# Performance work log

Measured on AMD Instinct MI355X. Metric: run time of the kernel, lower is better.

The kernel has to match this reference:

```python
import jax, jax.numpy as jnp
import numpy as np

HEADS = 8
DIM_HEAD = 64
SCALE = DIM_HEAD ** -0.5


def setup_inputs() -> dict:
    key = jax.random.key(0)
    k1, k2, k3 = jax.random.split(key, 3)
    b, dim, n = 4, 256, 2048
    hidden = HEADS * DIM_HEAD  # 512
    x = jax.random.normal(k1, (b, dim, n), dtype=jnp.float32)
    # Conv1d kernel-size-1 weights are pointwise linear maps over channels.
    w_qkv = jax.random.normal(k2, (3 * hidden, dim), dtype=jnp.float32) * (dim ** -0.5)
    w_out = jax.random.normal(k3, (dim, hidden), dtype=jnp.float32) * (hidden ** -0.5)
    b_out = jnp.zeros((dim,), dtype=jnp.float32)
    return {"x": x, "w_qkv": w_qkv, "w_out": w_out, "b_out": b_out}


def reference(x, w_qkv, w_out, b_out):
    b, dim, n = x.shape
    hidden = w_out.shape[1]
    # pointwise conv1d == channel matmul: [3h, dim] x [b, dim, n] -> [b, 3h, n]
    qkv = jnp.einsum('oi,bin->bon', w_qkv, x)
    q, k, v = jnp.split(qkv, 3, axis=1)
    # b (h c) n -> b h c n
    reshape = lambda t: t.reshape(b, HEADS, DIM_HEAD, n)
    q, k, v = reshape(q) * SCALE, reshape(k), reshape(v)
    sim = jnp.einsum('bhdi,bhdj->bhij', q, k)          # [b, h, n, n]
    attn = jax.nn.softmax(sim, axis=-1)
    out = jnp.einsum('bhij,bhdj->bhid', attn, v)        # [b, h, n, d]
    # b h n d -> b (h d) n
    out = out.transpose(0, 1, 3, 2).reshape(b, hidden, n)
    return jnp.einsum('oi,bin->bon', w_out, out) + b_out[None, :, None]
```

## Files before the change

### kernel.cpp

```cpp
#include <hip/hip_runtime.h>
#include <stdint.h>

#define SEQ  2048
#define DIMC 256
#define HID  512
#define NH   8
#define DH   64

typedef __attribute__((ext_vector_type(8))) short bf16x8;
typedef __attribute__((ext_vector_type(4))) float f32x4;
typedef __attribute__((ext_vector_type(16))) float f32x16;
typedef __attribute__((ext_vector_type(2))) unsigned uint2v;
typedef __attribute__((address_space(1))) const uint32_t guint_t;
typedef __attribute__((address_space(3))) uint32_t luint_t;

__device__ __forceinline__ void gld16(const void* g, void* l) {
  __builtin_amdgcn_global_load_lds((guint_t*)g, (luint_t*)l, 16, 0, 0);
}

__device__ __forceinline__ void barrier_raw() {
  asm volatile("" ::: "memory");
  __builtin_amdgcn_s_barrier();
  asm volatile("" ::: "memory");
}
#define WAITVM(n) asm volatile("s_waitcnt vmcnt(" #n ")" ::: "memory")

__device__ __forceinline__ unsigned short f2bf(float f) {
  union { float f; uint32_t u; } v; v.f = f;
  return (unsigned short)((v.u + 0x7FFFu + ((v.u >> 16) & 1u)) >> 16);
}

__device__ __forceinline__ uint32_t fbits(float f) {
  union { float f; uint32_t u; } v; v.f = f; return v.u;
}

__device__ __forceinline__ uint32_t pku(uint32_t u0, uint32_t u1) {
  return __builtin_amdgcn_perm(u1 + 0x8000u, u0 + 0x8000u, 0x07060302u);
}

__device__ __forceinline__ void swap32(uint32_t& a, uint32_t& b) {
#if __has_builtin(__builtin_amdgcn_permlane32_swap)
  uint2v r = __builtin_amdgcn_permlane32_swap(a, b, false, false);
  a = r[0]; b = r[1];
#else
  uint32_t aw = __shfl_xor(a, 32);
  uint32_t bw = __shfl_xor(b, 32);
  bool lo = (threadIdx.x & 32) == 0;
  uint32_t an = lo ? a : bw;
  uint32_t bn = lo ? aw : b;
  a = an; b = bn;
#endif
}

__global__ __launch_bounds__(256) void prep_kernel(
    const float* __restrict__ x, const float* __restrict__ wqkv,
    const float* __restrict__ wout,
    unsigned short* __restrict__ wqkv_b, unsigned short* __restrict__ wout_b,
    unsigned short* __restrict__ xT) {
  __shared__ float tile[64][65];
  int blk = blockIdx.x;
  int t = threadIdx.x;
  if (blk < 384) {
    int idx = blk * 1024 + t * 4;
    float4 v = *(const float4*)(wqkv + idx);
    float s = ((idx >> 8) < HID) ? 0.18033688011112042f : 1.0f;
    ushort4 o;
    o.x = f2bf(v.x * s); o.y = f2bf(v.y * s);
    o.z = f2bf(v.z * s); o.w = f2bf(v.w * s);
    *(ushort4*)(wqkv_b + idx) = o;
    return;
  }
  if (blk < 512) {
    int idx = (blk - 384) * 1024 + t * 4;
    float4 v = *(const float4*)(wout + idx);
    ushort4 o;
    o.x = f2bf(v.x); o.y = f2bf(v.y); o.z = f2bf(v.z); o.w = f2bf(v.w);
    *(ushort4*)(wout_b + idx) = o;
    return;
  }
  int tid = blk - 512;
  int b  = tid >> 7;
  int r  = tid & 127;
  int i0 = (r >> 5) * 64;
  int n0 = (r & 31) * 64;
  const float* xb = x + (size_t)b * DIMC * SEQ;
  int tn = t & 15, ti = t >> 4;
#pragma unroll
  for (int j = 0; j < 4; j++) {
    int il = ti + j * 16;
    float4 v = *(const float4*)(xb + (size_t)(i0 + il) * SEQ + n0 + tn * 4);
    tile[il][tn*4+0] = v.x; tile[il][tn*4+1] = v.y;
    tile[il][tn*4+2] = v.z; tile[il][tn*4+3] = v.w;
  }
  __syncthreads();
  unsigned short* xTb = xT + (size_t)b * SEQ * DIMC;
#pragma unroll
  for (int j = 0; j < 4; j++) {
    int nl = ti + j * 16;
    int i4 = tn * 4;
    uint2 pk;
    pk.x = (uint32_t)f2bf(tile[i4+0][nl]) | ((uint32_t)f2bf(tile[i4+1][nl]) << 16);
    pk.y = (uint32_t)f2bf(tile[i4+2][nl]) | ((uint32_t)f2bf(tile[i4+3][nl]) << 16);
    *(uint2*)(xTb + (size_t)(n0 + nl) * DIMC + i0 + i4) = pk;
  }
}

__global__ __launch_bounds__(256, 2) void qkv_gemm(
    const unsigned short* __restrict__ wq, const unsigned short* __restrict__ xT,
    unsigned short* __restrict__ Qs, unsigned short* __restrict__ Ks,
    unsigned short* __restrict__ Vt) {
  __shared__ unsigned short lds[32768];
  int o0 = blockIdx.x * 128;
  int n0 = blockIdx.y * 128;
  int b  = blockIdx.z;
  int t  = threadIdx.x;
  int wv = t >> 6, l = t & 63, l15 = l & 15, q = l >> 4;
  int wm = (wv & 1) * 64, wn = (wv >> 1) * 64;
  f32x4 acc[4][4];
#pragma unroll
  for (int i = 0; i < 4; i++)
#pragma unroll
    for (int j = 0; j < 4; j++) acc[i][j] = (f32x4){0.f, 0.f, 0.f, 0.f};
  const unsigned short* Ag = wq + (size_t)o0 * DIMC;
  const unsigned short* Bg = xT + ((size_t)b * SEQ + n0) * DIMC;
  int lrow8 = l >> 3, lcol = l & 7;

  auto stage = [&](int kk, int buf) {
    unsigned short* la = lds + (buf << 14);
    unsigned short* lb = la + 8192;
    int k0 = kk * 64;
#pragma unroll
    for (int c0 = 0; c0 < 4; c0++) {
      int c = wv * 4 + c0;
      int row = c * 8 + lrow8;
      int sg = lcol ^ (row & 7);
      gld16(Ag + (size_t)row * DIMC + k0 + sg * 8, la + c * 512);
      gld16(Bg + (size_t)row * DIMC + k0 + sg * 8, lb + c * 512);
    }
  };

  stage(0, 0);
  for (int kk = 0; kk < 4; kk++) {
    int cur = kk & 1;
    WAITVM(0);
    barrier_raw();
    if (kk < 3) stage(kk + 1, cur ^ 1);
    unsigned short* la = lds + (cur << 14);
    unsigned short* lb = la + 8192;
#pragma unroll
    for (int kh = 0; kh < 2; kh++) {
      bf16x8 af[4], bfr[4];
#pragma unroll
      for (int mt = 0; mt < 4; mt++) {
        int row = wm + mt*16 + l15;
        af[mt] = *(const bf16x8*)(la + row*64 + ((kh*4 + q) ^ (row & 7)) * 8);
      }
#pragma unroll
      for (int nt = 0; nt < 4; nt++) {
        int row = wn + nt*16 + l15;
        bfr[nt] = *(const bf16x8*)(lb + row*64 + ((kh*4 + q) ^ (row & 7)) * 8);
      }
#pragma unroll
      for (int mt = 0; mt < 4; mt++)
#pragma unroll
        for (int nt = 0; nt < 4; nt++)
          acc[mt][nt] = __builtin_amdgcn_mfma_f32_16x16x32_bf16(af[mt], bfr[nt], acc[mt][nt], 0, 0, 0);
    }
  }
  barrier_raw();
  int seg3 = o0 >> 9;
  int h0   = (o0 & 511) >> 6;
  if (seg3 == 2) {
#pragma unroll
    for (int mt = 0; mt < 4; mt++)
#pragma unroll
      for (int nt = 0; nt < 4; nt++)
#pragma unroll
        for (int r = 0; r < 4; r++) {
          int ol = wm + mt * 16 + q * 4 + r;
          int h = h0 + (ol >> 6), d = ol & 63;
          int n = n0 + wn + nt * 16 + l15;
          Vt[(((size_t)b * NH + h) * DH + d) * SEQ + n] = f2bf(acc[mt][nt][r]);
        }
  } else {
    unsigned short* dst = (seg3 == 0) ? Qs : Ks;
#pragma unroll
    for (int mt = 0; mt < 4; mt++)
#pragma unroll
      for (int nt = 0; nt < 4; nt++)
#pragma unroll
        for (int r = 0; r < 4; r++) {
          int ol = wm + mt * 16 + q * 4 + r;
          int nn = wn + nt * 16 + l15;
          lds[nn * 136 + ol] = f2bf(acc[mt][nt][r]);
        }
    __syncthreads();
#pragma unroll
    for (int i = 0; i < 8; i++) {
      int idx = i * 256 + t;
      int nn  = idx >> 4;
      int olb = (idx & 15) * 8;
      uint4 v = *(const uint4*)(lds + nn * 136 + olb);
      int h = h0 + (olb >> 6), d = olb & 63;
      *(uint4*)(dst + (((size_t)b * NH + h) * SEQ + n0 + nn) * DH + d) = v;
    }
  }
}

__global__ __launch_bounds__(256, 4) void attn_kernel(
    const unsigned short* __restrict__ Qs, const unsigned short* __restrict__ Ks,
    const unsigned short* __restrict__ Vt, unsigned short* __restrict__ AO) {
  __shared__ unsigned short KVs[16384];
  __shared__ float Lc[128];
  int id = blockIdx.x;
  int s  = id >> 3;
  int bh = (id & 7) * 4 + (s & 3);
  int q0 = (s >> 2) * 64;
  int b = bh >> 3, h = bh & 7;
  int t = threadIdx.x;
  int w = t >> 6, l = t & 63, l31 = l & 31, lh = l >> 5;
  int cg = w & 1, qg = w >> 1;
  const unsigned short* Qg = Qs + ((size_t)bh * SEQ + q0 + qg * 32) * DH;
  bf16x8 qb[4];
#pragma unroll
  for (int kc = 0; kc < 4; kc++)
    qb[kc] = *(const bf16x8*)(Qg + l31 * DH + kc*16 + lh*8);
  f32x16 oacc[2];
  float lsum = 0.f;
#pragma unroll
  for (int dt = 0; dt < 2; dt++)
#pragma unroll
    for (int r = 0; r < 16; r++) oacc[dt][r] = 0.f;

  const unsigned short* Ksrc = Ks + ((size_t)bh * SEQ + cg * 1024) * DH;
  const unsigned short* Vsrc = Vt + (size_t)bh * DH * SEQ + cg * 1024;

  auto stage = [&](int it2, int buf) {
    int jb = it2 * 32;
    unsigned short* base = KVs + buf * 8192;
    if (w < 2) {
      const unsigned short* src = Ksrc + (size_t)jb * DH;
      unsigned short* dst = base + cg * 2048;
#pragma unroll
      for (int g = 0; g < 4; g++) {
        int kr = g * 8 + (l >> 3);
        gld16(src + (size_t)kr * DH + ((l & 7) ^ (kr & 7)) * 8, dst + g * 512);
      }
    } else {
      const unsigned short* src = Vsrc + jb;
      unsigned short* dst = base + 4096 + cg * 2048;
#pragma unroll
      for (int g = 0; g < 4; g++) {
        int r = g * 8 + (l >> 3);
        int u = (l & 7) ^ (r & 7);
        int d = (u >> 2) * 32 + r;
        int j = u & 3;
        gld16(src + (size_t)d * SEQ + j * 8, dst + g * 512);
      }
    }
  };

  stage(0, 0);
  for (int it = 0; it < 32; it++) {
    int cur = it & 1;
    WAITVM(0);
    barrier_raw();
    if (it < 31) stage(it + 1, cur ^ 1);
    const unsigned short* Kst = KVs + cur * 8192 + cg * 2048;
    const unsigned short* Vst = KVs + cur * 8192 + 4096 + cg * 2048;
    f32x16 st;
#pragma unroll
    for (int r = 0; r < 16; r++) st[r] = 0.f;
#pragma unroll
    for (int kc = 0; kc < 4; kc++) {
      bf16x8 kf = *(const bf16x8*)(Kst + l31 * 64 + ((kc*2 + lh) ^ (l31 & 7)) * 8);
      st = __builtin_amdgcn_mfma_f32_32x32x16_bf16(kf, qb[kc], st, 0, 0, 0);
    }
    bf16x8 vf[2][2];
#pragma unroll
    for (int kc2 = 0; kc2 < 2; kc2++)
#pragma unroll
      for (int dt = 0; dt < 2; dt++)
        vf[kc2][dt] = *(const bf16x8*)(Vst + l31 * 64 +
                                       ((dt*4 + kc2*2 + lh) ^ (l31 & 7)) * 8);
    float p[16];
    float s0 = 0.f;
#pragma unroll
    for (int r = 0; r < 16; r++) { p[r] = __builtin_amdgcn_exp2f(st[r]); s0 += p[r]; }
    lsum += s0;
    bf16x8 af[2];
#pragma unroll
    for (int hf = 0; hf < 2; hf++) {
      uint32_t xs[4], ys[4];
#pragma unroll
      for (int j = 0; j < 4; j++) {
        xs[j] = fbits(p[hf*8 + j]);
        ys[j] = fbits(p[hf*8 + 4 + j]);
        swap32(xs[j], ys[j]);
      }
      uint32_t d0 = pku(xs[0], xs[1]);
      uint32_t d1 = pku(xs[2], xs[3]);
      uint32_t d2 = pku(ys[0], ys[1]);
      uint32_t d3 = pku(ys[2], ys[3]);
      union { uint32_t u[4]; bf16x8 v; } cv;
      cv.u[0] = d0; cv.u[1] = d1; cv.u[2] = d2; cv.u[3] = d3;
      af[hf] = cv.v;
    }
#pragma unroll
    for (int kc2 = 0; kc2 < 2; kc2++)
#pragma unroll
      for (int dt = 0; dt < 2; dt++)
        oacc[dt] = __builtin_amdgcn_mfma_f32_32x32x16_bf16(af[kc2], vf[kc2][dt], oacc[dt], 0, 0, 0);
  }
  {
    float v = lsum;
    v += __shfl_xor(v, 32);
    if (l < 32) Lc[cg * 64 + qg * 32 + l31] = v;
  }
  __syncthreads();
  float* Oc = (float*)KVs;
  if (cg == 1) {
#pragma unroll
    for (int dt = 0; dt < 2; dt++)
#pragma unroll
      for (int r = 0; r < 16; r++) {
        int qrow = qg*32 + (r & 3) + 8*(r >> 2) + 4*lh;
        Oc[qrow * 64 + dt*32 + l31] = oacc[dt][r];
      }
  }
  __syncthreads();
  if (cg == 0) {
    unsigned short* AOb = AO + (size_t)b * SEQ * HID + h * DH;
#pragma unroll
    for (int r = 0; r < 16; r++) {
      int qrow = qg*32 + (r & 3) + 8*(r >> 2) + 4*lh;
      float inv = __builtin_amdgcn_rcpf(Lc[qrow] + Lc[64 + qrow]);
      int n = q0 + qrow;
#pragma unroll
      for (int dt = 0; dt < 2; dt++) {
        float val = (oacc[dt][r] + Oc[qrow * 64 + dt*32 + l31]) * inv;
        AOb[(size_t)n * HID + dt*32 + l31] = f2bf(val);
      }
    }
  }
}

__global__ __launch_bounds__(256, 2) void out_gemm(
    const unsigned short* __restrict__ wo, const unsigned short* __restrict__ AO,
    const float* __restrict__ bias, float* __restrict__ out) {
  __shared__ unsigned short lds[24576];
  int o0 = blockIdx.x * 64;
  int n0 = blockIdx.y * 128;
  int b  = blockIdx.z;
  int t  = threadIdx.x;
  int wv = t >> 6, l = t & 63, l15 = l & 15, q = l >> 4;
  int wm = (wv & 1) * 32, wn = (wv >> 1) * 64;
  f32x4 acc[2][4];
#pragma unroll
  for (int i = 0; i < 2; i++)
#pragma unroll
    for (int j = 0; j < 4; j++) acc[i][j] = (f32x4){0.f,0.f,0.f,0.f};
  const unsigned short* Ag = wo + (size_t)o0 * HID;
  const unsigned short* Bg = AO + ((size_t)b * SEQ + n0) * HID;
  int lrow8 = l >> 3, lcol = l & 7;

  auto stage = [&](int kk, int buf) {
    unsigned short* la = lds + buf * 12288;
    unsigned short* lb = la + 4096;
    int k0 = kk * 64;
#pragma unroll
    for (int c0 = 0; c0 < 2; c0++) {
      int c = wv * 2 + c0;
      int row = c * 8 + lrow8;
      int sg = lcol ^ (row & 7);
      gld16(Ag + (size_t)row * HID + k0 + sg * 8, la + c * 512);
    }
#pragma unroll
    for (int c0 = 0; c0 < 4; c0++) {
      int c = wv * 4 + c0;
      int row = c * 8 + lrow8;
      int sg = lcol ^ (row & 7);
      gld16(Bg + (size_t)row * HID + k0 + sg * 8, lb + c * 512);
    }
  };

  stage(0, 0);
  for (int kk = 0; kk < 8; kk++) {
    int cur = kk & 1;
    WAITVM(0);
    barrier_raw();
    if (kk < 7) stage(kk + 1, cur ^ 1);
    unsigned short* la = lds + cur * 12288;
    unsigned short* lb = la + 4096;
#pragma unroll
    for (int kh = 0; kh < 2; kh++) {
      bf16x8 af[2], bfr[4];
#pragma unroll
      for (int mt = 0; mt < 2; mt++) {
        int row = wm + mt*16 + l15;
        af[mt] = *(const bf16x8*)(la + row*64 + ((kh*4 + q) ^ (row & 7)) * 8);
      }
#pragma unroll
      for (int nt = 0; nt < 4; nt++) {
        int row = wn + nt*16 + l15;
        bfr[nt] = *(const bf16x8*)(lb + row*64 + ((kh*4 + q) ^ (row & 7)) * 8);
      }
#pragma unroll
      for (int mt = 0; mt < 2; mt++)
#pragma unroll
        for (int nt = 0; nt < 4; nt++)
          acc[mt][nt] = __builtin_amdgcn_mfma_f32_16x16x32_bf16(af[mt], bfr[nt], acc[mt][nt], 0,0,0);
    }
  }
#pragma unroll
  for (int mt = 0; mt < 2; mt++)
#pragma unroll
    for (int nt = 0; nt < 4; nt++)
#pragma unroll
      for (int r = 0; r < 4; r++) {
        int o2 = o0 + wm + mt*16 + q*4 + r;
        int n  = n0 + wn + nt*16 + l15;
        out[((size_t)b * DIMC + o2) * SEQ + n] = acc[mt][nt][r] + bias[o2];
      }
}

extern "C" void kernel_launch(void* const* d_in, const int* in_sizes, int n_in,
                              void* d_out, int out_size, void* d_ws, size_t ws_size,
                              hipStream_t stream) {
  const float* x    = (const float*)d_in[0];
  const float* wqkv = (const float*)d_in[1];
  const float* wout = (const float*)d_in[2];
  const float* bout = (const float*)d_in[3];
  float* out = (float*)d_out;
  char* ws = (char*)d_ws;
  unsigned short* wqkv_b = (unsigned short*)(ws);
  unsigned short* wout_b = (unsigned short*)(ws + 786432);
  unsigned short* xT     = (unsigned short*)(ws + 1048576);
  unsigned short* Qs     = (unsigned short*)(ws + 5242880);
  unsigned short* Ks     = (unsigned short*)(ws + 13631488);
  unsigned short* Vt     = (unsigned short*)(ws + 22020096);
  unsigned short* AO     = (unsigned short*)(ws + 30408704);
  prep_kernel<<<1024, 256, 0, stream>>>(x, wqkv, wout, wqkv_b, wout_b, xT);
  qkv_gemm<<<dim3(12, 16, 4), 256, 0, stream>>>(wqkv_b, xT, Qs, Ks, Vt);
  attn_kernel<<<1024, 256, 0, stream>>>(Qs, Ks, Vt, AO);
  out_gemm<<<dim3(4, 16, 4), 256, 0, stream>>>(wout_b, AO, bout, out);
}
```

Before: 139.1 us.

## Tune attention inner loop, coalesce V stores, shrink out_gemm tiles

```diff
diff --git a/kernel.cpp b/kernel.cpp
--- a/kernel.cpp
+++ b/kernel.cpp
@@ -33,9 +33,14 @@
 __device__ __forceinline__ uint32_t fbits(float f) {
   union { float f; uint32_t u; } v; v.f = f; return v.u;
 }
-
-__device__ __forceinline__ uint32_t pku(uint32_t u0, uint32_t u1) {
-  return __builtin_amdgcn_perm(u1 + 0x8000u, u0 + 0x8000u, 0x07060302u);
+__device__ __forceinline__ float ffrombits(uint32_t u) {
+  union { uint32_t u; float f; } v; v.u = u; return v.f;
+}
+
+__device__ __forceinline__ uint32_t cvtpk(float a, float b) {
+  uint32_t r;
+  asm("v_cvt_pk_bf16_f32 %0, %1, %2" : "=v"(r) : "v"(a), "v"(b));
+  return r;
 }
 
 __device__ __forceinline__ void swap32(uint32_t& a, uint32_t& b) {
@@ -105,7 +110,7 @@
   }
 }
 
-__global__ __launch_bounds__(256, 2) void qkv_gemm(
+__global__ __launch_bounds__(256, 3) void qkv_gemm(
     const unsigned short* __restrict__ wq, const unsigned short* __restrict__ xT,
     unsigned short* __restrict__ Qs, unsigned short* __restrict__ Ks,
     unsigned short* __restrict__ Vt) {
@@ -178,10 +183,19 @@
 #pragma unroll
         for (int r = 0; r < 4; r++) {
           int ol = wm + mt * 16 + q * 4 + r;
-          int h = h0 + (ol >> 6), d = ol & 63;
-          int n = n0 + wn + nt * 16 + l15;
-          Vt[(((size_t)b * NH + h) * DH + d) * SEQ + n] = f2bf(acc[mt][nt][r]);
+          int nn = wn + nt * 16 + l15;
+          lds[ol * 136 + nn] = f2bf(acc[mt][nt][r]);
         }
+    __syncthreads();
+#pragma unroll
+    for (int i = 0; i < 8; i++) {
+      int idx = i * 256 + t;
+      int ol  = idx >> 4;
+      int nnb = (idx & 15) * 8;
+      uint4 v = *(const uint4*)(lds + ol * 136 + nnb);
+      int h = h0 + (ol >> 6), d = ol & 63;
+      *(uint4*)(Vt + (((size_t)b * NH + h) * DH + d) * SEQ + n0 + nnb) = v;
+    }
   } else {
     unsigned short* dst = (seg3 == 0) ? Qs : Ks;
 #pragma unroll
@@ -235,29 +249,36 @@
   const unsigned short* Ksrc = Ks + ((size_t)bh * SEQ + cg * 1024) * DH;
   const unsigned short* Vsrc = Vt + (size_t)bh * DH * SEQ + cg * 1024;
 
+  const unsigned short* sgp[4];
+  unsigned short* dst0;
+  size_t step;
+  if (w < 2) {
+#pragma unroll
+    for (int g = 0; g < 4; g++) {
+      int kr = g * 8 + (l >> 3);
+      sgp[g] = Ksrc + (size_t)kr * DH + ((l & 7) ^ (kr & 7)) * 8;
+    }
+    dst0 = (unsigned short*)KVs + cg * 2048;
+    step = (size_t)32 * DH;
+  } else {
+#pragma unroll
+    for (int g = 0; g < 4; g++) {
+      int r = g * 8 + (l >> 3);
+      int u = (l & 7) ^ (r & 7);
+      int d = (u >> 2) * 32 + r;
+      int j = u & 3;
+      sgp[g] = Vsrc + (size_t)d * SEQ + j * 8;
+    }
+    dst0 = (unsigned short*)KVs + 4096 + cg * 2048;
+    step = 32;
+  }
+
   auto stage = [&](int it2, int buf) {
-    int jb = it2 * 32;
-    unsigned short* base = KVs + buf * 8192;
-    if (w < 2) {
-      const unsigned short* src = Ksrc + (size_t)jb * DH;
-      unsigned short* dst = base + cg * 2048;
-#pragma unroll
-      for (int g = 0; g < 4; g++) {
-        int kr = g * 8 + (l >> 3);
-        gld16(src + (size_t)kr * DH + ((l & 7) ^ (kr & 7)) * 8, dst + g * 512);
-      }
-    } else {
-      const unsigned short* src = Vsrc + jb;
-      unsigned short* dst = base + 4096 + cg * 2048;
-#pragma unroll
-      for (int g = 0; g < 4; g++) {
-        int r = g * 8 + (l >> 3);
-        int u = (l & 7) ^ (r & 7);
-        int d = (u >> 2) * 32 + r;
-        int j = u & 3;
-        gld16(src + (size_t)d * SEQ + j * 8, dst + g * 512);
-      }
-    }
+    size_t off = (size_t)it2 * step;
+    unsigned short* dstb = dst0 + buf * 8192;
+#pragma unroll
+    for (int g = 0; g < 4; g++)
+      gld16(sgp[g] + off, dstb + g * 512);
   };
 
   stage(0, 0);
@@ -271,11 +292,13 @@
     f32x16 st;
 #pragma unroll
     for (int r = 0; r < 16; r++) st[r] = 0.f;
+    __builtin_amdgcn_s_setprio(1);
 #pragma unroll
     for (int kc = 0; kc < 4; kc++) {
       bf16x8 kf = *(const bf16x8*)(Kst + l31 * 64 + ((kc*2 + lh) ^ (l31 & 7)) * 8);
       st = __builtin_amdgcn_mfma_f32_32x32x16_bf16(kf, qb[kc], st, 0, 0, 0);
     }
+    __builtin_amdgcn_s_setprio(0);
     bf16x8 vf[2][2];
 #pragma unroll
     for (int kc2 = 0; kc2 < 2; kc2++)
@@ -284,10 +307,14 @@
         vf[kc2][dt] = *(const bf16x8*)(Vst + l31 * 64 +
                                        ((dt*4 + kc2*2 + lh) ^ (l31 & 7)) * 8);
     float p[16];
-    float s0 = 0.f;
-#pragma unroll
-    for (int r = 0; r < 16; r++) { p[r] = __builtin_amdgcn_exp2f(st[r]); s0 += p[r]; }
-    lsum += s0;
+#pragma unroll
+    for (int r = 0; r < 16; r++) p[r] = __builtin_amdgcn_exp2f(st[r]);
+    {
+      float t0 = p[0]+p[1],  t1 = p[2]+p[3],  t2 = p[4]+p[5],  t3 = p[6]+p[7];
+      float t4 = p[8]+p[9],  t5 = p[10]+p[11], t6 = p[12]+p[13], t7 = p[14]+p[15];
+      float u0 = t0+t1, u1 = t2+t3, u2 = t4+t5, u3 = t6+t7;
+      lsum += (u0+u1) + (u2+u3);
+    }
     bf16x8 af[2];
 #pragma unroll
     for (int hf = 0; hf < 2; hf++) {
@@ -298,19 +325,20 @@
         ys[j] = fbits(p[hf*8 + 4 + j]);
         swap32(xs[j], ys[j]);
       }
-      uint32_t d0 = pku(xs[0], xs[1]);
-      uint32_t d1 = pku(xs[2], xs[3]);
-      uint32_t d2 = pku(ys[0], ys[1]);
-      uint32_t d3 = pku(ys[2], ys[3]);
       union { uint32_t u[4]; bf16x8 v; } cv;
-      cv.u[0] = d0; cv.u[1] = d1; cv.u[2] = d2; cv.u[3] = d3;
+      cv.u[0] = cvtpk(ffrombits(xs[0]), ffrombits(xs[1]));
+      cv.u[1] = cvtpk(ffrombits(xs[2]), ffrombits(xs[3]));
+      cv.u[2] = cvtpk(ffrombits(ys[0]), ffrombits(ys[1]));
+      cv.u[3] = cvtpk(ffrombits(ys[2]), ffrombits(ys[3]));
       af[hf] = cv.v;
     }
+    __builtin_amdgcn_s_setprio(1);
 #pragma unroll
     for (int kc2 = 0; kc2 < 2; kc2++)
 #pragma unroll
       for (int dt = 0; dt < 2; dt++)
         oacc[dt] = __builtin_amdgcn_mfma_f32_32x32x16_bf16(af[kc2], vf[kc2][dt], oacc[dt], 0, 0, 0);
+    __builtin_amdgcn_s_setprio(0);
   }
   {
     float v = lsum;
@@ -348,24 +376,24 @@
 __global__ __launch_bounds__(256, 2) void out_gemm(
     const unsigned short* __restrict__ wo, const unsigned short* __restrict__ AO,
     const float* __restrict__ bias, float* __restrict__ out) {
-  __shared__ unsigned short lds[24576];
+  __shared__ unsigned short lds[16384];
   int o0 = blockIdx.x * 64;
-  int n0 = blockIdx.y * 128;
+  int n0 = blockIdx.y * 64;
   int b  = blockIdx.z;
   int t  = threadIdx.x;
   int wv = t >> 6, l = t & 63, l15 = l & 15, q = l >> 4;
-  int wm = (wv & 1) * 32, wn = (wv >> 1) * 64;
-  f32x4 acc[2][4];
+  int wm = (wv & 1) * 32, wn = (wv >> 1) * 32;
+  f32x4 acc[2][2];
 #pragma unroll
   for (int i = 0; i < 2; i++)
 #pragma unroll
-    for (int j = 0; j < 4; j++) acc[i][j] = (f32x4){0.f,0.f,0.f,0.f};
+    for (int j = 0; j < 2; j++) acc[i][j] = (f32x4){0.f,0.f,0.f,0.f};
   const unsigned short* Ag = wo + (size_t)o0 * HID;
   const unsigned short* Bg = AO + ((size_t)b * SEQ + n0) * HID;
   int lrow8 = l >> 3, lcol = l & 7;
 
   auto stage = [&](int kk, int buf) {
-    unsigned short* la = lds + buf * 12288;
+    unsigned short* la = lds + buf * 8192;
     unsigned short* lb = la + 4096;
     int k0 = kk * 64;
 #pragma unroll
@@ -374,12 +402,6 @@
       int row = c * 8 + lrow8;
       int sg = lcol ^ (row & 7);
       gld16(Ag + (size_t)row * HID + k0 + sg * 8, la + c * 512);
-    }
-#pragma unroll
-    for (int c0 = 0; c0 < 4; c0++) {
-      int c = wv * 4 + c0;
-      int row = c * 8 + lrow8;
-      int sg = lcol ^ (row & 7);
       gld16(Bg + (size_t)row * HID + k0 + sg * 8, lb + c * 512);
     }
   };
@@ -390,32 +412,32 @@
     WAITVM(0);
     barrier_raw();
     if (kk < 7) stage(kk + 1, cur ^ 1);
-    unsigned short* la = lds + cur * 12288;
+    unsigned short* la = lds + cur * 8192;
     unsigned short* lb = la + 4096;
 #pragma unroll
     for (int kh = 0; kh < 2; kh++) {
-      bf16x8 af[2], bfr[4];
+      bf16x8 af[2], bfr[2];
 #pragma unroll
       for (int mt = 0; mt < 2; mt++) {
         int row = wm + mt*16 + l15;
         af[mt] = *(const bf16x8*)(la + row*64 + ((kh*4 + q) ^ (row & 7)) * 8);
       }
 #pragma unroll
-      for (int nt = 0; nt < 4; nt++) {
+      for (int nt = 0; nt < 2; nt++) {
         int row = wn + nt*16 + l15;
         bfr[nt] = *(const bf16x8*)(lb + row*64 + ((kh*4 + q) ^ (row & 7)) * 8);
       }
 #pragma unroll
       for (int mt = 0; mt < 2; mt++)
 #pragma unroll
-        for (int nt = 0; nt < 4; nt++)
+        for (int nt = 0; nt < 2; nt++)
           acc[mt][nt] = __builtin_amdgcn_mfma_f32_16x16x32_bf16(af[mt], bfr[nt], acc[mt][nt], 0,0,0);
     }
   }
 #pragma unroll
   for (int mt = 0; mt < 2; mt++)
 #pragma unroll
-    for (int nt = 0; nt < 4; nt++)
+    for (int nt = 0; nt < 2; nt++)
 #pragma unroll
       for (int r = 0; r < 4; r++) {
         int o2 = o0 + wm + mt*16 + q*4 + r;
@@ -443,5 +465,5 @@
   prep_kernel<<<1024, 256, 0, stream>>>(x, wqkv, wout, wqkv_b, wout_b, xT);
   qkv_gemm<<<dim3(12, 16, 4), 256, 0, stream>>>(wqkv_b, xT, Qs, Ks, Vt);
   attn_kernel<<<1024, 256, 0, stream>>>(Qs, Ks, Vt, AO);
-  out_gemm<<<dim3(4, 16, 4), 256, 0, stream>>>(wout_b, AO, bout, out);
-}
+  out_gemm<<<dim3(4, 32, 4), 256, 0, stream>>>(wout_b, AO, bout, out);
+}
```

Measured after the change: 133.0 us. -4.3%, faster.
